# Performance work log

Hardware: AMD Instinct MI355X
Metric: run time of the kernel (lower is better)

Reference implementation:

```python
import jax, jax.numpy as jnp
import numpy as np


def setup_inputs() -> dict:
    key = jax.random.key(0)
    k1, k2, k3, k4 = jax.random.split(key, 4)
    B, T, C, H = 16, 2048, 1024, 128
    x = jax.random.normal(k1, (B, T, C), dtype=jnp.float32)
    # bias-free Dense kernels (stored as [in, out] like keras)
    s = 1.0 / np.sqrt(C)
    Wk = jax.random.normal(k2, (C, H), dtype=jnp.float32) * s
    Wq = jax.random.normal(k3, (C, H), dtype=jnp.float32) * s
    Wv = jax.random.normal(k4, (C, H), dtype=jnp.float32) * s
    return {"x": x, "Wk": Wk, "Wq": Wq, "Wv": Wv}


def reference(x, Wk, Wq, Wv):
    # single-head causal self-attention (dropout inactive at inference)
    B, T, C = x.shape
    H = Wk.shape[-1]
    k = jnp.einsum('btc,ch->bth', x, Wk)   # [B,T,H]
    q = jnp.einsum('btc,ch->bth', x, Wq)
    v = jnp.einsum('btc,ch->bth', x, Wv)
    scale = 1.0 / jnp.sqrt(jnp.float32(H))
    wei = jnp.einsum('bqh,bkh->bqk', q, k) * scale          # [B,T,T]
    causal = jnp.tril(jnp.ones((T, T), dtype=bool))
    wei = jnp.where(causal, wei, -jnp.inf)
    wei = jax.nn.softmax(wei, axis=-1)
    out = jnp.einsum('bqk,bkh->bqh', wei, v)                # [B,T,H]
    return out
```

## Files before the change

kernel.cpp:

```cpp
#include <hip/hip_runtime.h>
#include <hip/hip_bf16.h>

typedef __bf16 bf16x8_t __attribute__((ext_vector_type(8)));
typedef __bf16 bf16x4_t __attribute__((ext_vector_type(4)));
typedef float  f32x4_t  __attribute__((ext_vector_type(4)));

#define MFMA_16x16x32_BF16(A, B, C) __builtin_amdgcn_mfma_f32_16x16x32_bf16((A), (B), (C), 0, 0, 0)

static constexpr int B_ = 16;
static constexpr int T_ = 2048;
static constexpr int C_ = 1024;
static constexpr int H_ = 128;
static constexpr long M_ = (long)B_ * T_;

__device__ __forceinline__ void gload_lds16(const void* g, void* l)
{
    __builtin_amdgcn_global_load_lds(
        (const __attribute__((address_space(1))) void*)g,
        (__attribute__((address_space(3))) void*)l, 16, 0, 0);
}

__global__ __launch_bounds__(128) void wt_kernel(
    const float* __restrict__ Wq, const float* __restrict__ Wk,
    const float* __restrict__ Wv, __bf16* __restrict__ WT)
{
    const int z = blockIdx.y;
    const float* __restrict__ W = (z == 0) ? Wq : (z == 1) ? Wk : Wv;
    const int h  = threadIdx.x;
    const int c0 = blockIdx.x * 8;
    bf16x8_t v;
    #pragma unroll
    for (int j = 0; j < 8; ++j)
        v[j] = (__bf16)W[(c0 + j) * H_ + h];
    *(bf16x8_t*)&WT[((long)z * H_ + h) * C_ + c0] = v;
}

__global__ __launch_bounds__(512, 4) void proj_kernel(
    const float*  __restrict__ x,
    const __bf16* __restrict__ WT,
    __bf16* __restrict__ qo,
    __bf16* __restrict__ ko,
    __bf16* __restrict__ vo)
{
    __shared__ float  XS[2][64 * 32];
    __shared__ __bf16 WS[2][384 * 32];

    const int tid  = threadIdx.x;
    const int w    = tid >> 6;
    const int lane = tid & 63;
    const int m16  = lane & 15;
    const int quad = lane >> 4;
    const int mt2  = w >> 2;
    const int nq   = w & 3;

    const long r0 = (long)blockIdx.x * 64;

    const int xrow = tid >> 3;
    const int xcol = ((tid & 7) ^ (xrow & 7)) << 2;
    const int wrr  = lane >> 2;
    const int wqc  = ((lane & 3) ^ ((lane >> 3) & 3)) << 3;

    f32x4_t acc[2][6];
    #pragma unroll
    for (int hh = 0; hh < 2; ++hh)
        #pragma unroll
        for (int j = 0; j < 6; ++j) acc[hh][j] = f32x4_t{0, 0, 0, 0};

    gload_lds16(&x[(r0 + xrow) * C_ + xcol], &XS[0][w * 8 * 32]);
    #pragma unroll
    for (int ch = 0; ch < 3; ++ch) {
        const int rowb = w * 48 + ch * 16;
        gload_lds16(&WT[(long)(rowb + wrr) * C_ + wqc], &WS[0][rowb * 32]);
    }

    for (int t = 0; t < 32; ++t) {
        const int cur = t & 1, nxt = cur ^ 1;
        const int k0n = (t + 1) * 32;

        if (t < 31) {
            gload_lds16(&x[(r0 + xrow) * C_ + k0n + xcol], &XS[nxt][w * 8 * 32]);
            #pragma unroll
            for (int ch = 0; ch < 3; ++ch) {
                const int rowb = w * 48 + ch * 16;
                gload_lds16(&WT[(long)(rowb + wrr) * C_ + k0n + wqc],
                            &WS[nxt][rowb * 32]);
            }
            __builtin_amdgcn_sched_barrier(0);
            asm volatile("s_waitcnt vmcnt(4)" ::: "memory");
        } else {
            __builtin_amdgcn_sched_barrier(0);
            asm volatile("s_waitcnt vmcnt(0)" ::: "memory");
        }
        __builtin_amdgcn_s_barrier();
        __builtin_amdgcn_sched_barrier(0);

        bf16x8_t a[2];
        #pragma unroll
        for (int hh = 0; hh < 2; ++hh) {
            const int row = mt2 * 32 + hh * 16 + m16;
            const int sw  = m16 & 7;
            f32x4_t lo = *(const f32x4_t*)&XS[cur][row * 32 + (((quad * 2 + 0) ^ sw) << 2)];
            f32x4_t hi = *(const f32x4_t*)&XS[cur][row * 32 + (((quad * 2 + 1) ^ sw) << 2)];
            #pragma unroll
            for (int jj = 0; jj < 4; ++jj) {
                a[hh][jj]     = (__bf16)lo[jj];
                a[hh][4 + jj] = (__bf16)hi[jj];
            }
        }
        const int qsw = (quad ^ ((m16 >> 1) & 3)) << 3;
        #pragma unroll
        for (int j = 0; j < 6; ++j) {
            const int row = (nq * 6 + j) * 16 + m16;
            bf16x8_t b = *(const bf16x8_t*)&WS[cur][row * 32 + qsw];
            acc[0][j] = MFMA_16x16x32_BF16(a[0], b, acc[0][j]);
            acc[1][j] = MFMA_16x16x32_BF16(a[1], b, acc[1][j]);
        }

        __builtin_amdgcn_sched_barrier(0);
        asm volatile("s_waitcnt lgkmcnt(0)" ::: "memory");
        __builtin_amdgcn_s_barrier();
        __builtin_amdgcn_sched_barrier(0);
    }

    #pragma unroll
    for (int hh = 0; hh < 2; ++hh) {
        const long rbase = r0 + mt2 * 32 + hh * 16 + quad * 4;
        #pragma unroll
        for (int j = 0; j < 6; ++j) {
            const int nt = nq * 6 + j;
            const int z  = nt >> 3;
            const int h  = (nt & 7) * 16 + m16;
            if (z < 2) {
                __bf16* __restrict__ o = z ? ko : qo;
                #pragma unroll
                for (int r = 0; r < 4; ++r)
                    o[(rbase + r) * H_ + h] = (__bf16)acc[hh][j][r];
            } else {
                long bb = rbase >> 11, tt = rbase & 2047;
                bf16x4_t pk;
                #pragma unroll
                for (int r = 0; r < 4; ++r) pk[r] = (__bf16)acc[hh][j][r];
                *(bf16x4_t*)&vo[bb * (H_ * (long)T_) + h * (long)T_ + tt] = pk;
            }
        }
    }
}

__global__ __launch_bounds__(256) void attn_kernel(
    const __bf16* __restrict__ q,
    const __bf16* __restrict__ k,
    const __bf16* __restrict__ vT,
    float* __restrict__ out)
{
    __shared__ __bf16 KS[64 * 136];
    __shared__ __bf16 VS[128 * 72];
    __shared__ __bf16 PS[4][16 * 72];

    const int L   = blockIdx.x;
    const int b   = L & 15;
    const int Lh  = L >> 4;
    const int qb  = (Lh < 16) ? (31 - Lh) : (Lh - 16);

    const int tid  = threadIdx.x;
    const int w    = tid >> 6;
    const int lane = tid & 63;
    const int m16  = lane & 15;
    const int quad = lane >> 4;
    const int koff = quad * 8;

    const __bf16* __restrict__ qp = q  + (long)b * T_ * H_;
    const __bf16* __restrict__ kp = k  + (long)b * T_ * H_;
    const __bf16* __restrict__ vp = vT + (long)b * H_ * T_;

    const int q0w = qb * 64 + w * 16;
    const int qg  = q0w + m16;

    bf16x8_t qfr[4];
    #pragma unroll
    for (int s = 0; s < 4; ++s)
        qfr[s] = *(const bf16x8_t*)&qp[(q0w + m16) * H_ + s * 32 + koff];

    f32x4_t acc[8];
    #pragma unroll
    for (int i = 0; i < 8; ++i) acc[i] = f32x4_t{0, 0, 0, 0};
    float mrun = -1e30f, lrun = 0.f;

    __bf16* Pb = &PS[w][0];
    const float SC = 0.08838834764831845f;
    const int kend = qb * 64 + 64;

    const int krow = tid >> 4, kc16 = tid & 15;
    const int vrow = tid >> 3, vc8  = tid & 7;

    for (int tk0 = 0; tk0 < kend; tk0 += 64) {
        __syncthreads();
        #pragma unroll
        for (int ch = 0; ch < 4; ++ch) {
            int r = krow + ch * 16;
            *(bf16x8_t*)&KS[r * 136 + kc16 * 8] =
                *(const bf16x8_t*)&kp[(tk0 + r) * H_ + kc16 * 8];
        }
        #pragma unroll
        for (int ch = 0; ch < 4; ++ch) {
            int hh = vrow + ch * 32;
            *(bf16x8_t*)&VS[hh * 72 + vc8 * 8] =
                *(const bf16x8_t*)&vp[hh * (long)T_ + tk0 + vc8 * 8];
        }
        __syncthreads();

        f32x4_t st[4];
        #pragma unroll
        for (int kt = 0; kt < 4; ++kt) {
            f32x4_t s = f32x4_t{0, 0, 0, 0};
            #pragma unroll
            for (int sI = 0; sI < 4; ++sI) {
                bf16x8_t kf = *(const bf16x8_t*)&KS[(kt * 16 + m16) * 136 + sI * 32 + koff];
                s = MFMA_16x16x32_BF16(kf, qfr[sI], s);
            }
            st[kt] = s;
        }

        float vv[4][4];
        if (tk0 + 63 <= q0w) {
            #pragma unroll
            for (int kt = 0; kt < 4; ++kt)
                #pragma unroll
                for (int r = 0; r < 4; ++r)
                    vv[kt][r] = st[kt][r] * SC;
        } else {
            #pragma unroll
            for (int kt = 0; kt < 4; ++kt)
                #pragma unroll
                for (int r = 0; r < 4; ++r) {
                    int kg = tk0 + kt * 16 + quad * 4 + r;
                    vv[kt][r] = (kg <= qg) ? st[kt][r] * SC : -1e30f;
                }
        }

        float mloc = -1e30f;
        #pragma unroll
        for (int kt = 0; kt < 4; ++kt)
            #pragma unroll
            for (int r = 0; r < 4; ++r)
                mloc = fmaxf(mloc, vv[kt][r]);
        mloc = fmaxf(mloc, __shfl_xor(mloc, 16, 64));
        mloc = fmaxf(mloc, __shfl_xor(mloc, 32, 64));

        float mnew = fmaxf(mrun, mloc);
        float al   = __expf(mrun - mnew);
        float psum = 0.f;
        #pragma unroll
        for (int kt = 0; kt < 4; ++kt) {
            bf16x4_t pk;
            #pragma unroll
            for (int r = 0; r < 4; ++r) {
                float p = __expf(vv[kt][r] - mnew);
                psum += p;
                pk[r] = (__bf16)p;
            }
            *(bf16x4_t*)&Pb[m16 * 72 + kt * 16 + quad * 4] = pk;
        }
        psum += __shfl_xor(psum, 16, 64);
        psum += __shfl_xor(psum, 32, 64);
        mrun = mnew;
        lrun = lrun * al + psum;

        #pragma unroll
        for (int i = 0; i < 8; ++i)
            #pragma unroll
            for (int r = 0; r < 4; ++r)
                acc[i][r] *= al;

        #pragma unroll
        for (int half = 0; half < 2; ++half) {
            bf16x8_t pa = *(const bf16x8_t*)&Pb[m16 * 72 + half * 32 + koff];
            #pragma unroll
            for (int i = 0; i < 8; ++i) {
                bf16x8_t vf = *(const bf16x8_t*)&VS[(i * 16 + m16) * 72 + half * 32 + koff];
                acc[i] = MFMA_16x16x32_BF16(vf, pa, acc[i]);
            }
        }
    }

    float* __restrict__ ob = out + (long)b * T_ * H_;
    const float inv = 1.f / lrun;
    #pragma unroll
    for (int i = 0; i < 8; ++i) {
        f32x4_t o;
        #pragma unroll
        for (int r = 0; r < 4; ++r) o[r] = acc[i][r] * inv;
        *(f32x4_t*)&ob[(q0w + m16) * H_ + i * 16 + quad * 4] = o;
    }
}

extern "C" void kernel_launch(void* const* d_in, const int* in_sizes, int n_in,
                              void* d_out, int out_size, void* d_ws, size_t ws_size,
                              hipStream_t stream)
{
    const float* x  = (const float*)d_in[0];
    const float* Wk = (const float*)d_in[1];
    const float* Wq = (const float*)d_in[2];
    const float* Wv = (const float*)d_in[3];

    __bf16* qws = (__bf16*)d_ws;
    __bf16* kws = qws + M_ * H_;
    __bf16* vws = kws + M_ * H_;
    __bf16* WT  = vws + (long)B_ * H_ * T_;
    float*  out = (float*)d_out;

    wt_kernel  <<<dim3(C_ / 8, 3), 128, 0, stream>>>(Wq, Wk, Wv, WT);
    proj_kernel<<<dim3((int)(M_ / 64)), 512, 0, stream>>>(x, WT, qws, kws, vws);
    attn_kernel<<<dim3(512), 256, 0, stream>>>(qws, kws, vws, out);
}
```

Before: 290.6 us.

## Double projection M-tile to 128 rows with triple-buffered LDS pipeline

The projection kernel now covers 128 rows of x per block instead of 64, so each weight tile loaded into LDS feeds twice as many MFMAs and total weight traffic is halved. The LDS ring grows from two to three buffers, with loads issued two k-steps ahead and a vmcnt wait placed after the MFMAs, giving memory latency more time to hide. Each wave now holds 4x6 accumulators, and the occupancy hint drops from 4 to 2 blocks per SM, with more LDS per block. The cost is fewer resident waves and higher register pressure.

```diff
diff --git a/kernel.cpp b/kernel.cpp
--- a/kernel.cpp
+++ b/kernel.cpp
@@ -35,99 +35,105 @@
     *(bf16x8_t*)&WT[((long)z * H_ + h) * C_ + c0] = v;
 }
 
-__global__ __launch_bounds__(512, 4) void proj_kernel(
+__global__ __launch_bounds__(512, 2) void proj_kernel(
     const float*  __restrict__ x,
     const __bf16* __restrict__ WT,
     __bf16* __restrict__ qo,
     __bf16* __restrict__ ko,
     __bf16* __restrict__ vo)
 {
-    __shared__ float  XS[2][64 * 32];
-    __shared__ __bf16 WS[2][384 * 32];
+    __shared__ float  XS[3][128 * 32];
+    __shared__ __bf16 WS[3][384 * 32];
 
     const int tid  = threadIdx.x;
     const int w    = tid >> 6;
     const int lane = tid & 63;
     const int m16  = lane & 15;
     const int quad = lane >> 4;
-    const int mt2  = w >> 2;
-    const int nq   = w & 3;
-
-    const long r0 = (long)blockIdx.x * 64;
-
-    const int xrow = tid >> 3;
-    const int xcol = ((tid & 7) ^ (xrow & 7)) << 2;
-    const int wrr  = lane >> 2;
-    const int wqc  = ((lane & 3) ^ ((lane >> 3) & 3)) << 3;
-
-    f32x4_t acc[2][6];
-    #pragma unroll
-    for (int hh = 0; hh < 2; ++hh)
+    const int wm   = w >> 2;
+    const int wn   = w & 3;
+
+    const long r0 = (long)blockIdx.x * 128;
+
+    const int xl_row = lane >> 3;
+    const int xl_u   = (lane & 7) ^ xl_row;
+    const int wl_row = lane >> 2;
+    const int wl_u   = (lane & 3) ^ ((lane >> 3) & 3);
+
+    f32x4_t acc[4][6];
+    #pragma unroll
+    for (int hh = 0; hh < 4; ++hh)
         #pragma unroll
         for (int j = 0; j < 6; ++j) acc[hh][j] = f32x4_t{0, 0, 0, 0};
 
-    gload_lds16(&x[(r0 + xrow) * C_ + xcol], &XS[0][w * 8 * 32]);
-    #pragma unroll
-    for (int ch = 0; ch < 3; ++ch) {
-        const int rowb = w * 48 + ch * 16;
-        gload_lds16(&WT[(long)(rowb + wrr) * C_ + wqc], &WS[0][rowb * 32]);
-    }
+#define ISSUE(T, BUF)                                                        \
+    {                                                                        \
+        const int k0_ = (T) * 32;                                            \
+        _Pragma("unroll")                                                    \
+        for (int ch = 0; ch < 2; ++ch) {                                     \
+            const int rb = w * 8 + ch * 64;                                  \
+            gload_lds16(&x[(r0 + rb + xl_row) * C_ + k0_ + xl_u * 4],        \
+                        &XS[BUF][rb * 32]);                                  \
+        }                                                                    \
+        _Pragma("unroll")                                                    \
+        for (int ch = 0; ch < 3; ++ch) {                                     \
+            const int rb = w * 48 + ch * 16;                                 \
+            gload_lds16(&WT[(long)(rb + wl_row) * C_ + k0_ + wl_u * 8],      \
+                        &WS[BUF][rb * 32]);                                  \
+        }                                                                    \
+    }
+
+    ISSUE(0, 0);
+    ISSUE(1, 1);
+    asm volatile("s_waitcnt vmcnt(5)" ::: "memory");
+    __builtin_amdgcn_sched_barrier(0);
+    __builtin_amdgcn_s_barrier();
+    __builtin_amdgcn_sched_barrier(0);
+
+    const int asw = m16 & 7;
+    const int qsw = (quad ^ ((m16 >> 1) & 3)) << 3;
 
     for (int t = 0; t < 32; ++t) {
-        const int cur = t & 1, nxt = cur ^ 1;
-        const int k0n = (t + 1) * 32;
-
-        if (t < 31) {
-            gload_lds16(&x[(r0 + xrow) * C_ + k0n + xcol], &XS[nxt][w * 8 * 32]);
-            #pragma unroll
-            for (int ch = 0; ch < 3; ++ch) {
-                const int rowb = w * 48 + ch * 16;
-                gload_lds16(&WT[(long)(rowb + wrr) * C_ + k0n + wqc],
-                            &WS[nxt][rowb * 32]);
-            }
-            __builtin_amdgcn_sched_barrier(0);
-            asm volatile("s_waitcnt vmcnt(4)" ::: "memory");
-        } else {
-            __builtin_amdgcn_sched_barrier(0);
-            asm volatile("s_waitcnt vmcnt(0)" ::: "memory");
-        }
-        __builtin_amdgcn_s_barrier();
+        const int cur = t % 3;
+        if (t + 2 < 32) ISSUE(t + 2, (t + 2) % 3);
         __builtin_amdgcn_sched_barrier(0);
 
-        bf16x8_t a[2];
-        #pragma unroll
-        for (int hh = 0; hh < 2; ++hh) {
-            const int row = mt2 * 32 + hh * 16 + m16;
-            const int sw  = m16 & 7;
-            f32x4_t lo = *(const f32x4_t*)&XS[cur][row * 32 + (((quad * 2 + 0) ^ sw) << 2)];
-            f32x4_t hi = *(const f32x4_t*)&XS[cur][row * 32 + (((quad * 2 + 1) ^ sw) << 2)];
+        bf16x8_t a[4];
+        #pragma unroll
+        for (int hh = 0; hh < 4; ++hh) {
+            const int row = wm * 64 + hh * 16 + m16;
+            f32x4_t lo = *(const f32x4_t*)&XS[cur][row * 32 + (((quad * 2 + 0) ^ asw) << 2)];
+            f32x4_t hi = *(const f32x4_t*)&XS[cur][row * 32 + (((quad * 2 + 1) ^ asw) << 2)];
             #pragma unroll
             for (int jj = 0; jj < 4; ++jj) {
                 a[hh][jj]     = (__bf16)lo[jj];
                 a[hh][4 + jj] = (__bf16)hi[jj];
             }
         }
-        const int qsw = (quad ^ ((m16 >> 1) & 3)) << 3;
         #pragma unroll
         for (int j = 0; j < 6; ++j) {
-            const int row = (nq * 6 + j) * 16 + m16;
+            const int row = wn * 96 + j * 16 + m16;
             bf16x8_t b = *(const bf16x8_t*)&WS[cur][row * 32 + qsw];
-            acc[0][j] = MFMA_16x16x32_BF16(a[0], b, acc[0][j]);
-            acc[1][j] = MFMA_16x16x32_BF16(a[1], b, acc[1][j]);
+            #pragma unroll
+            for (int hh = 0; hh < 4; ++hh)
+                acc[hh][j] = MFMA_16x16x32_BF16(a[hh], b, acc[hh][j]);
         }
 
         __builtin_amdgcn_sched_barrier(0);
+        if (t + 2 < 32) asm volatile("s_waitcnt vmcnt(5)" ::: "memory");
+        else            asm volatile("s_waitcnt vmcnt(0)" ::: "memory");
         asm volatile("s_waitcnt lgkmcnt(0)" ::: "memory");
         __builtin_amdgcn_s_barrier();
         __builtin_amdgcn_sched_barrier(0);
     }
-
-    #pragma unroll
-    for (int hh = 0; hh < 2; ++hh) {
-        const long rbase = r0 + mt2 * 32 + hh * 16 + quad * 4;
+#undef ISSUE
+
+    #pragma unroll
+    for (int hh = 0; hh < 4; ++hh) {
+        const long rbase = r0 + wm * 64 + hh * 16 + quad * 4;
         #pragma unroll
         for (int j = 0; j < 6; ++j) {
-            const int nt = nq * 6 + j;
+            const int nt = wn * 6 + j;
             const int z  = nt >> 3;
             const int h  = (nt & 7) * 16 + m16;
             if (z < 2) {
@@ -309,6 +315,6 @@
     float*  out = (float*)d_out;
 
     wt_kernel  <<<dim3(C_ / 8, 3), 128, 0, stream>>>(Wq, Wk, Wv, WT);
-    proj_kernel<<<dim3((int)(M_ / 64)), 512, 0, stream>>>(x, WT, qws, kws, vws);
+    proj_kernel<<<dim3((int)(M_ / 128)), 512, 0, stream>>>(x, WT, qws, kws, vws);
     attn_kernel<<<dim3(512), 256, 0, stream>>>(qws, kws, vws, out);
 }
```

New measurement: 276.5 us. -4.9%, faster.
